# Performance work log

Measured on AMD Instinct MI355X. Metric: run time of the kernel, lower is better.

Reference implementation:

```python
import jax, jax.numpy as jnp
import numpy as np

# dims: B=batch, CIN/COUT=channels, T=timesteps, K=kernel length (= T+1, since
# max_timesteps=2048 is even and CKConv bumps it to odd), DK=SIREN hidden width
B, CIN, COUT, T, DK = 32, 32, 32, 2048, 32
K = T + 1


def setup_inputs() -> dict:
    key = jax.random.key(0)
    ks = jax.random.split(key, 9)
    u = lambda k, shape, lim: jax.random.uniform(k, shape, minval=-lim, maxval=lim)
    # SIREN layer 1 (Conv1d 1->DK, k=1): first layer init uniform(-1, 1)
    w1 = u(ks[0], (DK, 1), 1.0)
    b1 = u(ks[1], (DK,), 1.0)          # torch bias init: U(-1/sqrt(fan_in)), fan_in=1
    # SIREN layer 2 (DK->DK): uniform(-sqrt(6/DK)/omega0, +), omega0=1
    siren_val = float(np.sqrt(6.0 / DK))
    w2 = u(ks[2], (DK, DK), siren_val)
    b2 = u(ks[3], (DK,), float(1.0 / np.sqrt(DK)))
    # output layer (DK -> CIN*COUT)
    w3 = u(ks[4], (CIN * COUT, DK), siren_val)
    b3 = u(ks[5], (CIN * COUT,), float(1.0 / np.sqrt(DK)))
    omega1 = jnp.asarray(1.0, jnp.float32)
    omega2 = jnp.asarray(1.0, jnp.float32)
    bias = jax.random.normal(ks[6], (COUT,), jnp.float32)   # CKConv output bias
    x = jax.random.normal(ks[7], (B, CIN, T), jnp.float32)
    rel_pos = jnp.linspace(-1.0, 1.0, K, dtype=jnp.float32)  # buffer _rel_positions
    return dict(x=x, rel_pos=rel_pos, w1=w1, b1=b1, omega1=omega1,
                w2=w2, b2=b2, omega2=omega2, w3=w3, b3=b3, bias=bias)


def reference(x, rel_pos, w1, b1, omega1, w2, b2, omega2, w3, b3, bias):
    # --- SIREN kernel network: 1x1 convs over the K positions == matmuls ---
    pos = rel_pos[None, :]                                   # (1, K)
    h = jnp.sin(omega1 * (w1 @ pos + b1[:, None]))           # (DK, K)
    h = jnp.sin(omega2 * (w2 @ h + b2[:, None]))             # (DK, K)
    kern = (w3 @ h + b3[:, None]).reshape(COUT, CIN, K)      # (COUT, CIN, K)
    # --- causal conv: left-pad by K-1 zeros, then valid cross-correlation ---
    out = jax.lax.conv_general_dilated(
        x, kern, window_strides=(1,), padding=[(K - 1, 0)],
        dimension_numbers=("NCH", "OIH", "NCH"))             # (B, COUT, T)
    return out + bias[None, :, None]
```

## Files before the change

### kernel.cpp

```cpp
#include <hip/hip_runtime.h>
#include <hip/hip_bf16.h>
#include <stdint.h>

typedef short bf16x8 __attribute__((ext_vector_type(8)));
typedef float f32x16 __attribute__((ext_vector_type(16)));

#define T 2048
#define KLEN 2049
#define DK 32
#define NCO 32
#define NCI 32
#define NB 32

#define GR 2216
#define SREF 2055
#define WT_CH 257
#define WT_ELEMS (NCI*WT_CH*NCO*8)
#define XR_ELEMS (NB*NCI*GR)

#define WT_OFF 0
#define XR_OFF (WT_ELEMS*2)
#define XRS_OFF (XR_OFF + XR_ELEMS*2)

#define CIB 400
#define CPYB 13376
#define BUFB 27264
#define RED_OFF (2*BUFB)
#define LDS_TOT (RED_OFF + 16384)

__global__ __launch_bounds__(256) void gen_w(
    const float* __restrict__ rel_pos,
    const float* __restrict__ w1, const float* __restrict__ b1, const float* __restrict__ om1,
    const float* __restrict__ w2, const float* __restrict__ b2, const float* __restrict__ om2,
    const float* __restrict__ w3, const float* __restrict__ b3,
    uint16_t* __restrict__ Wt)
{
    int d = blockIdx.x;
    int tid = threadIdx.x;
    if (d >= KLEN) {
        for (int r = 0; r < 4; ++r) {
            int coci = tid + 256*r;
            int co = coci >> 5, ci = coci & 31;
            Wt[(((ci*WT_CH + (d>>3))*NCO + co)<<3) + (d&7)] = 0;
        }
        return;
    }
    int kk = 2048 - d;
    float pos = rel_pos[kk];
    __shared__ float h1[DK];
    __shared__ float h2[DK];
    if (tid < DK) h1[tid] = sinf(om1[0]*(w1[tid]*pos + b1[tid]));
    __syncthreads();
    if (tid < DK) {
        float a = b2[tid];
        for (int j = 0; j < DK; ++j) a += w2[tid*DK+j]*h1[j];
        h2[tid] = sinf(om2[0]*a);
    }
    __syncthreads();
    for (int r = 0; r < 4; ++r) {
        int coci = tid + 256*r;
        float a = b3[coci];
        for (int j = 0; j < DK; ++j) a += w3[coci*DK+j]*h2[j];
        int co = coci >> 5, ci = coci & 31;
        __hip_bfloat16 hv = __float2bfloat16(a);
        Wt[(((ci*WT_CH + (d>>3))*NCO + co)<<3) + (d&7)] = *(uint16_t*)&hv;
    }
}

__global__ __launch_bounds__(256) void gen_x(const float* __restrict__ x,
                                             uint16_t* __restrict__ xr,
                                             uint16_t* __restrict__ xrs)
{
    int idx = blockIdx.x*256 + threadIdx.x;
    if (idx >= NB*NCI*GR) return;
    int row = idx / GR;
    int g = idx - row*GR;
    int s = SREF - g;
    float v  = (s  >= 0 && s  < T) ? x[row*T + s]  : 0.f;
    int s2 = s - 1;
    float v2 = (s2 >= 0 && s2 < T) ? x[row*T + s2] : 0.f;
    __hip_bfloat16 hv = __float2bfloat16(v);
    __hip_bfloat16 hv2 = __float2bfloat16(v2);
    xr[idx]  = *(uint16_t*)&hv;
    xrs[idx] = *(uint16_t*)&hv2;
}

__device__ __forceinline__ void gld16(const uint16_t* g, char* l)
{
    typedef const __attribute__((address_space(1))) uint32_t GU;
    typedef __attribute__((address_space(3))) uint32_t LU;
    __builtin_amdgcn_global_load_lds((GU*)g, (LU*)l, 16, 0, 0);
}

__global__ __launch_bounds__(512, 2) void conv(
    const uint16_t* __restrict__ Wt, const uint16_t* __restrict__ xr,
    const float* __restrict__ bias, float* __restrict__ out)
{
    __shared__ uint4 lds4[LDS_TOT/16];
    char* ldsb = (char*)lds4;
    float* red = (float*)(ldsb + RED_OFF);
    int tid = threadIdx.x;
    int p = blockIdx.x >> 5;
    int b = blockIdx.x & 31;
    int w = tid >> 6, lane = tid & 63, n = lane & 31, hi = lane >> 5;
    int cig = w;

    int srcE[4], dstC[4];
    #pragma unroll
    for (int k = 0; k < 4; ++k) {
        int idxbase = (k < 3) ? (k*512 + w*64) : (1536 + w*64);
        int cpy = idxbase >= 832;
        int j0 = idxbase - cpy*832;
        dstC[k] = cpy*CPYB + (j0 << 4);
        int j = j0 + lane;
        if (j < 800) {
            int ci = (j*2622) >> 16;
            int q  = j - ci*25;
            srcE[k] = (cpy ? XR_ELEMS : 0) + (b*NCI + ci)*GR + (q << 3);
        } else srcE[k] = 0;
    }

    int obase = 39 - n + (hi << 3);
    int par = obase & 1;
    int bbb = cig*CIB + par*CPYB + ((obase - par) << 1);

    for (int phase = 0; phase < 2; ++phase) {
        int th = phase ? (63 - (p << 2)) : ((p << 2) + 3);
        int u = (th - 1) >> 1;
        int g0base = 2016 - (th << 5);

        f32x16 acc0, acc1, acc2, acc3;
        #pragma unroll
        for (int r = 0; r < 16; ++r) { acc0[r]=0.f; acc1[r]=0.f; acc2[r]=0.f; acc3[r]=0.f; }

        #pragma unroll
        for (int k = 0; k < 3; ++k)
            gld16(xr + srcE[k] + g0base, ldsb + dstC[k]);
        if (w < 2)
            gld16(xr + srcE[3] + g0base, ldsb + dstC[3]);
        __syncthreads();

        for (int wi = 0; wi <= u; ++wi) {
            int cur = wi & 1;
            if (wi < u) {
                int g0n = g0base + ((wi + 1) << 6);
                char* bufn = ldsb + (cur ^ 1)*BUFB;
                #pragma unroll
                for (int k = 0; k < 3; ++k)
                    gld16(xr + srcE[k] + g0n, bufn + dstC[k]);
                if (w < 2)
                    gld16(xr + srcE[3] + g0n, bufn + dstC[3]);
            }
            bool full = (wi < u);
            int dcw = wi << 3;
            const char* rbase = ldsb + cur*BUFB + bbb;

            #pragma unroll
            for (int cii = 0; cii < 4; ++cii) {
                int ci = (cii << 3) + cig;
                const uint16_t* aB = Wt + (((ci*WT_CH + dcw + hi)*NCO + n) << 3);
                bf16x8 av0 = *(const bf16x8*)(aB);
                bf16x8 av1 = *(const bf16x8*)(aB + 512);
                bf16x8 av2 = *(const bf16x8*)(aB + 1024);
                bf16x8 av3 = *(const bf16x8*)(aB + 1536);
                const char* pbase = rbase + cii*(8*CIB);

                #define RDBB(MM) union { uint32_t u_[4]; bf16x8 v; } bb; { \
                    const char* pp = pbase + ((MM) << 5); \
                    bb.u_[0] = *(const uint32_t*)(pp); \
                    bb.u_[1] = *(const uint32_t*)(pp + 4); \
                    bb.u_[2] = *(const uint32_t*)(pp + 8); \
                    bb.u_[3] = *(const uint32_t*)(pp + 12); }

                { RDBB(0) acc0 = __builtin_amdgcn_mfma_f32_32x32x16_bf16(av0, bb.v, acc0, 0,0,0); }
                { RDBB(1) acc0 = __builtin_amdgcn_mfma_f32_32x32x16_bf16(av1, bb.v, acc0, 0,0,0); }
                { RDBB(2) acc0 = __builtin_amdgcn_mfma_f32_32x32x16_bf16(av2, bb.v, acc0, 0,0,0);
                          acc1 = __builtin_amdgcn_mfma_f32_32x32x16_bf16(av0, bb.v, acc1, 0,0,0); }
                { RDBB(3) acc0 = __builtin_amdgcn_mfma_f32_32x32x16_bf16(av3, bb.v, acc0, 0,0,0);
                          acc1 = __builtin_amdgcn_mfma_f32_32x32x16_bf16(av1, bb.v, acc1, 0,0,0); }
                { RDBB(4) acc1 = __builtin_amdgcn_mfma_f32_32x32x16_bf16(av2, bb.v, acc1, 0,0,0);
                  if (full) acc2 = __builtin_amdgcn_mfma_f32_32x32x16_bf16(av0, bb.v, acc2, 0,0,0); }
                { RDBB(5) acc1 = __builtin_amdgcn_mfma_f32_32x32x16_bf16(av3, bb.v, acc1, 0,0,0);
                  if (full) acc2 = __builtin_amdgcn_mfma_f32_32x32x16_bf16(av1, bb.v, acc2, 0,0,0); }
                if (full) {
                    { RDBB(6) acc2 = __builtin_amdgcn_mfma_f32_32x32x16_bf16(av2, bb.v, acc2, 0,0,0);
                              acc3 = __builtin_amdgcn_mfma_f32_32x32x16_bf16(av0, bb.v, acc3, 0,0,0); }
                    { RDBB(7) acc2 = __builtin_amdgcn_mfma_f32_32x32x16_bf16(av3, bb.v, acc2, 0,0,0);
                              acc3 = __builtin_amdgcn_mfma_f32_32x32x16_bf16(av1, bb.v, acc3, 0,0,0); }
                    { RDBB(8) acc3 = __builtin_amdgcn_mfma_f32_32x32x16_bf16(av2, bb.v, acc3, 0,0,0); }
                    { RDBB(9) acc3 = __builtin_amdgcn_mfma_f32_32x32x16_bf16(av3, bb.v, acc3, 0,0,0); }
                }
                #undef RDBB
            }
            __syncthreads();
        }

        #pragma unroll
        for (int dlt = 0; dlt < 4; ++dlt) {
            f32x16 a = (dlt == 0) ? acc0 : (dlt == 1) ? acc1 : (dlt == 2) ? acc2 : acc3;
            __syncthreads();
            if (w < 4) {
                #pragma unroll
                for (int r = 0; r < 16; ++r)
                    red[(w*16 + r)*64 + lane] = a[r];
            }
            __syncthreads();
            if (w >= 4) {
                #pragma unroll
                for (int r = 0; r < 16; ++r)
                    red[((w-4)*16 + r)*64 + lane] += a[r];
            }
            __syncthreads();
            int t0 = (th - dlt) << 5;
            #pragma unroll
            for (int h = 0; h < 2; ++h) {
                int e = tid + (h << 9);
                int lane_e = e & 63;
                int reg = e >> 6;
                float s = 0.f;
                #pragma unroll
                for (int ww = 0; ww < 4; ++ww) s += red[(ww*16 + reg)*64 + lane_e];
                int co = (reg & 3) + ((reg >> 2) << 3) + ((lane_e >> 5) << 2);
                int t = t0 + (lane_e & 31);
                out[(b*NCO + co)*T + t] = s + bias[co];
            }
        }
        __syncthreads();
    }
}

extern "C" void kernel_launch(void* const* d_in, const int* in_sizes, int n_in,
                              void* d_out, int out_size, void* d_ws, size_t ws_size,
                              hipStream_t stream)
{
    const float* x       = (const float*)d_in[0];
    const float* rel_pos = (const float*)d_in[1];
    const float* w1  = (const float*)d_in[2];
    const float* b1  = (const float*)d_in[3];
    const float* om1 = (const float*)d_in[4];
    const float* w2  = (const float*)d_in[5];
    const float* b2  = (const float*)d_in[6];
    const float* om2 = (const float*)d_in[7];
    const float* w3  = (const float*)d_in[8];
    const float* b3  = (const float*)d_in[9];
    const float* bias = (const float*)d_in[10];
    float* out = (float*)d_out;
    char* ws = (char*)d_ws;
    uint16_t* Wt  = (uint16_t*)(ws + WT_OFF);
    uint16_t* xrp = (uint16_t*)(ws + XR_OFF);
    uint16_t* xrs = (uint16_t*)(ws + XRS_OFF);

    hipLaunchKernelGGL(gen_w, dim3(WT_CH*8), dim3(256), 0, stream,
                       rel_pos, w1, b1, om1, w2, b2, om2, w3, b3, Wt);
    int n2 = NB*NCI*GR;
    hipLaunchKernelGGL(gen_x, dim3((n2+255)/256), dim3(256), 0, stream, x, xrp, xrs);
    hipLaunchKernelGGL(conv, dim3(NB*8), dim3(512), 0, stream, Wt, xrp, bias, out);
}
```

Before: 179.6 us.

## Split conv phases into separate blocks and prefetch next weight fragments

Each block used to handle two time tiles (a short and a long one) in sequence. Now each phase is its own block, which doubles the grid to 512 blocks, and launch bounds rise to 4 blocks per SM to allow higher occupancy. Inside the inner loop, the A-operand weight loads for the next input-channel group are issued before the current MFMA chain to hide global latency. The price is more register pressure under the tighter launch bound, possible spills, and load imbalance, since each block's work now differs widely with its time position.

```diff
diff --git a/kernel.cpp b/kernel.cpp
--- a/kernel.cpp
+++ b/kernel.cpp
@@ -92,7 +92,7 @@
     __builtin_amdgcn_global_load_lds((GU*)g, (LU*)l, 16, 0, 0);
 }
 
-__global__ __launch_bounds__(512, 2) void conv(
+__global__ __launch_bounds__(512, 4) void conv(
     const uint16_t* __restrict__ Wt, const uint16_t* __restrict__ xr,
     const float* __restrict__ bias, float* __restrict__ out)
 {
@@ -100,8 +100,12 @@
     char* ldsb = (char*)lds4;
     float* red = (float*)(ldsb + RED_OFF);
     int tid = threadIdx.x;
-    int p = blockIdx.x >> 5;
     int b = blockIdx.x & 31;
+    int q = blockIdx.x >> 5;
+    int p = q & 7;
+    int th = (q < 8) ? (63 - (p << 2)) : ((p << 2) + 3);
+    int u = (th - 1) >> 1;
+    int g0base = 2016 - (th << 5);
     int w = tid >> 6, lane = tid & 63, n = lane & 31, hi = lane >> 5;
     int cig = w;
 
@@ -115,8 +119,8 @@
         int j = j0 + lane;
         if (j < 800) {
             int ci = (j*2622) >> 16;
-            int q  = j - ci*25;
-            srcE[k] = (cpy ? XR_ELEMS : 0) + (b*NCI + ci)*GR + (q << 3);
+            int qq = j - ci*25;
+            srcE[k] = (cpy ? XR_ELEMS : 0) + (b*NCI + ci)*GR + (qq << 3);
         } else srcE[k] = 0;
     }
 
@@ -124,108 +128,111 @@
     int par = obase & 1;
     int bbb = cig*CIB + par*CPYB + ((obase - par) << 1);
 
-    for (int phase = 0; phase < 2; ++phase) {
-        int th = phase ? (63 - (p << 2)) : ((p << 2) + 3);
-        int u = (th - 1) >> 1;
-        int g0base = 2016 - (th << 5);
-
-        f32x16 acc0, acc1, acc2, acc3;
+    f32x16 acc0, acc1, acc2, acc3;
+    #pragma unroll
+    for (int r = 0; r < 16; ++r) { acc0[r]=0.f; acc1[r]=0.f; acc2[r]=0.f; acc3[r]=0.f; }
+
+    #pragma unroll
+    for (int k = 0; k < 3; ++k)
+        gld16(xr + srcE[k] + g0base, ldsb + dstC[k]);
+    if (w < 2)
+        gld16(xr + srcE[3] + g0base, ldsb + dstC[3]);
+    __syncthreads();
+
+    for (int wi = 0; wi <= u; ++wi) {
+        int cur = wi & 1;
+        if (wi < u) {
+            int g0n = g0base + ((wi + 1) << 6);
+            char* bufn = ldsb + (cur ^ 1)*BUFB;
+            #pragma unroll
+            for (int k = 0; k < 3; ++k)
+                gld16(xr + srcE[k] + g0n, bufn + dstC[k]);
+            if (w < 2)
+                gld16(xr + srcE[3] + g0n, bufn + dstC[3]);
+        }
+        bool full = (wi < u);
+        int dcw = wi << 3;
+        const char* rbase = ldsb + cur*BUFB + bbb;
+
+        bf16x8 av0, av1, av2, av3, nv0, nv1, nv2, nv3;
+        {
+            const uint16_t* aB = Wt + (((cig*WT_CH + dcw + hi)*NCO + n) << 3);
+            av0 = *(const bf16x8*)(aB);
+            av1 = *(const bf16x8*)(aB + 512);
+            av2 = *(const bf16x8*)(aB + 1024);
+            av3 = *(const bf16x8*)(aB + 1536);
+        }
         #pragma unroll
-        for (int r = 0; r < 16; ++r) { acc0[r]=0.f; acc1[r]=0.f; acc2[r]=0.f; acc3[r]=0.f; }
-
+        for (int cii = 0; cii < 4; ++cii) {
+            if (cii < 3) {
+                const uint16_t* aN = Wt + (((((cii+1)*8 + cig)*WT_CH + dcw + hi)*NCO + n) << 3);
+                nv0 = *(const bf16x8*)(aN);
+                nv1 = *(const bf16x8*)(aN + 512);
+                nv2 = *(const bf16x8*)(aN + 1024);
+                nv3 = *(const bf16x8*)(aN + 1536);
+            }
+            const char* pbase = rbase + cii*(8*CIB);
+
+            #define RDBB(MM) union { uint32_t u_[4]; bf16x8 v; } bb; { \
+                const char* pp = pbase + ((MM) << 5); \
+                bb.u_[0] = *(const uint32_t*)(pp); \
+                bb.u_[1] = *(const uint32_t*)(pp + 4); \
+                bb.u_[2] = *(const uint32_t*)(pp + 8); \
+                bb.u_[3] = *(const uint32_t*)(pp + 12); }
+
+            { RDBB(0) acc0 = __builtin_amdgcn_mfma_f32_32x32x16_bf16(av0, bb.v, acc0, 0,0,0); }
+            { RDBB(1) acc0 = __builtin_amdgcn_mfma_f32_32x32x16_bf16(av1, bb.v, acc0, 0,0,0); }
+            { RDBB(2) acc0 = __builtin_amdgcn_mfma_f32_32x32x16_bf16(av2, bb.v, acc0, 0,0,0);
+                      acc1 = __builtin_amdgcn_mfma_f32_32x32x16_bf16(av0, bb.v, acc1, 0,0,0); }
+            { RDBB(3) acc0 = __builtin_amdgcn_mfma_f32_32x32x16_bf16(av3, bb.v, acc0, 0,0,0);
+                      acc1 = __builtin_amdgcn_mfma_f32_32x32x16_bf16(av1, bb.v, acc1, 0,0,0); }
+            { RDBB(4) acc1 = __builtin_amdgcn_mfma_f32_32x32x16_bf16(av2, bb.v, acc1, 0,0,0);
+              if (full) acc2 = __builtin_amdgcn_mfma_f32_32x32x16_bf16(av0, bb.v, acc2, 0,0,0); }
+            { RDBB(5) acc1 = __builtin_amdgcn_mfma_f32_32x32x16_bf16(av3, bb.v, acc1, 0,0,0);
+              if (full) acc2 = __builtin_amdgcn_mfma_f32_32x32x16_bf16(av1, bb.v, acc2, 0,0,0); }
+            if (full) {
+                { RDBB(6) acc2 = __builtin_amdgcn_mfma_f32_32x32x16_bf16(av2, bb.v, acc2, 0,0,0);
+                          acc3 = __builtin_amdgcn_mfma_f32_32x32x16_bf16(av0, bb.v, acc3, 0,0,0); }
+                { RDBB(7) acc2 = __builtin_amdgcn_mfma_f32_32x32x16_bf16(av3, bb.v, acc2, 0,0,0);
+                          acc3 = __builtin_amdgcn_mfma_f32_32x32x16_bf16(av1, bb.v, acc3, 0,0,0); }
+                { RDBB(8) acc3 = __builtin_amdgcn_mfma_f32_32x32x16_bf16(av2, bb.v, acc3, 0,0,0); }
+                { RDBB(9) acc3 = __builtin_amdgcn_mfma_f32_32x32x16_bf16(av3, bb.v, acc3, 0,0,0); }
+            }
+            #undef RDBB
+            if (cii < 3) { av0 = nv0; av1 = nv1; av2 = nv2; av3 = nv3; }
+        }
+        __syncthreads();
+    }
+
+    #pragma unroll
+    for (int dlt = 0; dlt < 4; ++dlt) {
+        f32x16 a = (dlt == 0) ? acc0 : (dlt == 1) ? acc1 : (dlt == 2) ? acc2 : acc3;
+        __syncthreads();
+        if (w < 4) {
+            #pragma unroll
+            for (int r = 0; r < 16; ++r)
+                red[(w*16 + r)*64 + lane] = a[r];
+        }
+        __syncthreads();
+        if (w >= 4) {
+            #pragma unroll
+            for (int r = 0; r < 16; ++r)
+                red[((w-4)*16 + r)*64 + lane] += a[r];
+        }
+        __syncthreads();
+        int t0 = (th - dlt) << 5;
         #pragma unroll
-        for (int k = 0; k < 3; ++k)
-            gld16(xr + srcE[k] + g0base, ldsb + dstC[k]);
-        if (w < 2)
-            gld16(xr + srcE[3] + g0base, ldsb + dstC[3]);
-        __syncthreads();
-
-        for (int wi = 0; wi <= u; ++wi) {
-            int cur = wi & 1;
-            if (wi < u) {
-                int g0n = g0base + ((wi + 1) << 6);
-                char* bufn = ldsb + (cur ^ 1)*BUFB;
-                #pragma unroll
-                for (int k = 0; k < 3; ++k)
-                    gld16(xr + srcE[k] + g0n, bufn + dstC[k]);
-                if (w < 2)
-                    gld16(xr + srcE[3] + g0n, bufn + dstC[3]);
-            }
-            bool full = (wi < u);
-            int dcw = wi << 3;
-            const char* rbase = ldsb + cur*BUFB + bbb;
-
-            #pragma unroll
-            for (int cii = 0; cii < 4; ++cii) {
-                int ci = (cii << 3) + cig;
-                const uint16_t* aB = Wt + (((ci*WT_CH + dcw + hi)*NCO + n) << 3);
-                bf16x8 av0 = *(const bf16x8*)(aB);
-                bf16x8 av1 = *(const bf16x8*)(aB + 512);
-                bf16x8 av2 = *(const bf16x8*)(aB + 1024);
-                bf16x8 av3 = *(const bf16x8*)(aB + 1536);
-                const char* pbase = rbase + cii*(8*CIB);
-
-                #define RDBB(MM) union { uint32_t u_[4]; bf16x8 v; } bb; { \
-                    const char* pp = pbase + ((MM) << 5); \
-                    bb.u_[0] = *(const uint32_t*)(pp); \
-                    bb.u_[1] = *(const uint32_t*)(pp + 4); \
-                    bb.u_[2] = *(const uint32_t*)(pp + 8); \
-                    bb.u_[3] = *(const uint32_t*)(pp + 12); }
-
-                { RDBB(0) acc0 = __builtin_amdgcn_mfma_f32_32x32x16_bf16(av0, bb.v, acc0, 0,0,0); }
-                { RDBB(1) acc0 = __builtin_amdgcn_mfma_f32_32x32x16_bf16(av1, bb.v, acc0, 0,0,0); }
-                { RDBB(2) acc0 = __builtin_amdgcn_mfma_f32_32x32x16_bf16(av2, bb.v, acc0, 0,0,0);
-                          acc1 = __builtin_amdgcn_mfma_f32_32x32x16_bf16(av0, bb.v, acc1, 0,0,0); }
-                { RDBB(3) acc0 = __builtin_amdgcn_mfma_f32_32x32x16_bf16(av3, bb.v, acc0, 0,0,0);
-                          acc1 = __builtin_amdgcn_mfma_f32_32x32x16_bf16(av1, bb.v, acc1, 0,0,0); }
-                { RDBB(4) acc1 = __builtin_amdgcn_mfma_f32_32x32x16_bf16(av2, bb.v, acc1, 0,0,0);
-                  if (full) acc2 = __builtin_amdgcn_mfma_f32_32x32x16_bf16(av0, bb.v, acc2, 0,0,0); }
-                { RDBB(5) acc1 = __builtin_amdgcn_mfma_f32_32x32x16_bf16(av3, bb.v, acc1, 0,0,0);
-                  if (full) acc2 = __builtin_amdgcn_mfma_f32_32x32x16_bf16(av1, bb.v, acc2, 0,0,0); }
-                if (full) {
-                    { RDBB(6) acc2 = __builtin_amdgcn_mfma_f32_32x32x16_bf16(av2, bb.v, acc2, 0,0,0);
-                              acc3 = __builtin_amdgcn_mfma_f32_32x32x16_bf16(av0, bb.v, acc3, 0,0,0); }
-                    { RDBB(7) acc2 = __builtin_amdgcn_mfma_f32_32x32x16_bf16(av3, bb.v, acc2, 0,0,0);
-                              acc3 = __builtin_amdgcn_mfma_f32_32x32x16_bf16(av1, bb.v, acc3, 0,0,0); }
-                    { RDBB(8) acc3 = __builtin_amdgcn_mfma_f32_32x32x16_bf16(av2, bb.v, acc3, 0,0,0); }
-                    { RDBB(9) acc3 = __builtin_amdgcn_mfma_f32_32x32x16_bf16(av3, bb.v, acc3, 0,0,0); }
-                }
-                #undef RDBB
-            }
-            __syncthreads();
-        }
-
-        #pragma unroll
-        for (int dlt = 0; dlt < 4; ++dlt) {
-            f32x16 a = (dlt == 0) ? acc0 : (dlt == 1) ? acc1 : (dlt == 2) ? acc2 : acc3;
-            __syncthreads();
-            if (w < 4) {
-                #pragma unroll
-                for (int r = 0; r < 16; ++r)
-                    red[(w*16 + r)*64 + lane] = a[r];
-            }
-            __syncthreads();
-            if (w >= 4) {
-                #pragma unroll
-                for (int r = 0; r < 16; ++r)
-                    red[((w-4)*16 + r)*64 + lane] += a[r];
-            }
-            __syncthreads();
-            int t0 = (th - dlt) << 5;
-            #pragma unroll
-            for (int h = 0; h < 2; ++h) {
-                int e = tid + (h << 9);
-                int lane_e = e & 63;
-                int reg = e >> 6;
-                float s = 0.f;
-                #pragma unroll
-                for (int ww = 0; ww < 4; ++ww) s += red[(ww*16 + reg)*64 + lane_e];
-                int co = (reg & 3) + ((reg >> 2) << 3) + ((lane_e >> 5) << 2);
-                int t = t0 + (lane_e & 31);
-                out[(b*NCO + co)*T + t] = s + bias[co];
-            }
-        }
-        __syncthreads();
+        for (int h = 0; h < 2; ++h) {
+            int e = tid + (h << 9);
+            int lane_e = e & 63;
+            int reg = e >> 6;
+            float s = 0.f;
+            #pragma unroll
+            for (int ww = 0; ww < 4; ++ww) s += red[(ww*16 + reg)*64 + lane_e];
+            int co = (reg & 3) + ((reg >> 2) << 3) + ((lane_e >> 5) << 2);
+            int t = t0 + (lane_e & 31);
+            out[(b*NCO + co)*T + t] = s + bias[co];
+        }
     }
 }
 
@@ -254,5 +261,5 @@
                        rel_pos, w1, b1, om1, w2, b2, om2, w3, b3, Wt);
     int n2 = NB*NCI*GR;
     hipLaunchKernelGGL(gen_x, dim3((n2+255)/256), dim3(256), 0, stream, x, xrp, xrs);
-    hipLaunchKernelGGL(conv, dim3(NB*8), dim3(512), 0, stream, Wt, xrp, bias, out);
-}
+    hipLaunchKernelGGL(conv, dim3(NB*16), dim3(512), 0, stream, Wt, xrp, bias, out);
+}
```

After: 181.5 us. No clear change (+1.1%).

## Widen causal-conv K-window per stage and split phases into separate blocks

Applied to the files above, without the earlier changes.

The conv kernel now stages twice the lag window per pipeline step (128 instead of 64 positions, 8 weight fragments per ci) and reuses each A fragment across four accumulator tiles with a longer MFMA chain. The two triangular phases that used to run sequentially in one block now go to separate blocks, doubling the grid to 512. The reduction buffer aliases the staging LDS, and launch bounds ask for 4 blocks per CU. The aim is fewer barriers and loop iterations per MFMA and more parallelism. The cost is a larger LDS footprint, more VGPR pressure from the extra A fragments, and some wasted MFMAs on the partial last window.

```diff
diff --git a/kernel.cpp b/kernel.cpp
--- a/kernel.cpp
+++ b/kernel.cpp
@@ -22,11 +22,12 @@
 #define XR_OFF (WT_ELEMS*2)
 #define XRS_OFF (XR_OFF + XR_ELEMS*2)
 
-#define CIB 400
-#define CPYB 13376
-#define BUFB 27264
-#define RED_OFF (2*BUFB)
-#define LDS_TOT (RED_OFF + 16384)
+#define CIB 528
+#define GPC 1056
+#define GPCP 1088
+#define CPYB 17472
+#define BUFB (2*CPYB)
+#define LDS_TOT (2*BUFB)
 
 __global__ __launch_bounds__(256) void gen_w(
     const float* __restrict__ rel_pos,
@@ -92,140 +93,137 @@
     __builtin_amdgcn_global_load_lds((GU*)g, (LU*)l, 16, 0, 0);
 }
 
-__global__ __launch_bounds__(512, 2) void conv(
+__global__ __launch_bounds__(512, 4) void conv(
     const uint16_t* __restrict__ Wt, const uint16_t* __restrict__ xr,
     const float* __restrict__ bias, float* __restrict__ out)
 {
     __shared__ uint4 lds4[LDS_TOT/16];
     char* ldsb = (char*)lds4;
-    float* red = (float*)(ldsb + RED_OFF);
+    float* red = (float*)lds4;
     int tid = threadIdx.x;
-    int p = blockIdx.x >> 5;
     int b = blockIdx.x & 31;
+    int q = blockIdx.x >> 5;
+    int p = q & 7;
+    int th = (q < 8) ? (63 - (p << 2)) : ((p << 2) + 3);
+    int nw = (th + 1) >> 2;
+    int g0base = 2016 - (th << 5);
     int w = tid >> 6, lane = tid & 63, n = lane & 31, hi = lane >> 5;
     int cig = w;
 
-    int srcE[4], dstC[4];
+    int srcE[5], dstC[5];
     #pragma unroll
-    for (int k = 0; k < 4; ++k) {
-        int idxbase = (k < 3) ? (k*512 + w*64) : (1536 + w*64);
-        int cpy = idxbase >= 832;
-        int j0 = idxbase - cpy*832;
-        dstC[k] = cpy*CPYB + (j0 << 4);
-        int j = j0 + lane;
-        if (j < 800) {
-            int ci = (j*2622) >> 16;
-            int q  = j - ci*25;
-            srcE[k] = (cpy ? XR_ELEMS : 0) + (b*NCI + ci)*GR + (q << 3);
-        } else srcE[k] = 0;
+    for (int k = 0; k < 5; ++k) {
+        int gi = tid + (k << 9);
+        if (gi < 2176) {
+            int cpy = gi >= GPCP;
+            int j = gi - cpy*GPCP;
+            dstC[k] = cpy*CPYB + (j << 4);
+            if (j < GPC) {
+                int ci = (j*1986) >> 16;
+                int qq = j - ci*33;
+                srcE[k] = (cpy ? XR_ELEMS : 0) + (b*NCI + ci)*GR + (qq << 3);
+            } else srcE[k] = 0;
+        } else { srcE[k] = 0; dstC[k] = -1; }
     }
 
     int obase = 39 - n + (hi << 3);
     int par = obase & 1;
     int bbb = cig*CIB + par*CPYB + ((obase - par) << 1);
 
-    for (int phase = 0; phase < 2; ++phase) {
-        int th = phase ? (63 - (p << 2)) : ((p << 2) + 3);
-        int u = (th - 1) >> 1;
-        int g0base = 2016 - (th << 5);
-
-        f32x16 acc0, acc1, acc2, acc3;
+    f32x16 acc0, acc1, acc2, acc3;
+    #pragma unroll
+    for (int r = 0; r < 16; ++r) { acc0[r]=0.f; acc1[r]=0.f; acc2[r]=0.f; acc3[r]=0.f; }
+
+    #define STAGE(BUF, GOFF) { \
+        _Pragma("unroll") \
+        for (int k = 0; k < 5; ++k) \
+            if (dstC[k] >= 0) gld16(xr + srcE[k] + (GOFF), (BUF) + dstC[k]); }
+
+    STAGE(ldsb, g0base)
+    __syncthreads();
+
+    for (int wi = 0; wi < nw; ++wi) {
+        int cur = wi & 1;
+        if (wi + 1 < nw) {
+            char* bufn = ldsb + (cur ^ 1)*BUFB;
+            int g0n = g0base + ((wi + 1) << 7);
+            STAGE(bufn, g0n)
+        }
+        int dcw = wi << 4;
+        const char* rbase = ldsb + cur*BUFB + bbb;
+
         #pragma unroll
-        for (int r = 0; r < 16; ++r) { acc0[r]=0.f; acc1[r]=0.f; acc2[r]=0.f; acc3[r]=0.f; }
-
+        for (int cii = 0; cii < 4; ++cii) {
+            int ci = (cii << 3) + cig;
+            const uint16_t* aB = Wt + (((ci*WT_CH + dcw + hi)*NCO + n) << 3);
+            bf16x8 av0 = *(const bf16x8*)(aB);
+            bf16x8 av1 = *(const bf16x8*)(aB + 512);
+            bf16x8 av2 = *(const bf16x8*)(aB + 1024);
+            bf16x8 av3 = *(const bf16x8*)(aB + 1536);
+            bf16x8 av4 = *(const bf16x8*)(aB + 2048);
+            bf16x8 av5 = *(const bf16x8*)(aB + 2560);
+            bf16x8 av6 = *(const bf16x8*)(aB + 3072);
+            bf16x8 av7 = *(const bf16x8*)(aB + 3584);
+            const char* pbase = rbase + cii*(8*CIB);
+
+            #define RDBB(MM) union { uint32_t u_[4]; bf16x8 v; } bb; { \
+                const char* pp = pbase + ((MM) << 5); \
+                bb.u_[0] = *(const uint32_t*)(pp); \
+                bb.u_[1] = *(const uint32_t*)(pp + 4); \
+                bb.u_[2] = *(const uint32_t*)(pp + 8); \
+                bb.u_[3] = *(const uint32_t*)(pp + 12); }
+            #define MF(AC, AV) AC = __builtin_amdgcn_mfma_f32_32x32x16_bf16(AV, bb.v, AC, 0,0,0);
+
+            { RDBB(0)  MF(acc0, av0) }
+            { RDBB(1)  MF(acc0, av1) }
+            { RDBB(2)  MF(acc0, av2) MF(acc1, av0) }
+            { RDBB(3)  MF(acc0, av3) MF(acc1, av1) }
+            { RDBB(4)  MF(acc0, av4) MF(acc1, av2) MF(acc2, av0) }
+            { RDBB(5)  MF(acc0, av5) MF(acc1, av3) MF(acc2, av1) }
+            { RDBB(6)  MF(acc0, av6) MF(acc1, av4) MF(acc2, av2) MF(acc3, av0) }
+            { RDBB(7)  MF(acc0, av7) MF(acc1, av5) MF(acc2, av3) MF(acc3, av1) }
+            { RDBB(8)  MF(acc1, av6) MF(acc2, av4) MF(acc3, av2) }
+            { RDBB(9)  MF(acc1, av7) MF(acc2, av5) MF(acc3, av3) }
+            { RDBB(10) MF(acc2, av6) MF(acc3, av4) }
+            { RDBB(11) MF(acc2, av7) MF(acc3, av5) }
+            { RDBB(12) MF(acc3, av6) }
+            { RDBB(13) MF(acc3, av7) }
+            #undef MF
+            #undef RDBB
+        }
+        __syncthreads();
+    }
+    #undef STAGE
+
+    #pragma unroll
+    for (int dlt = 0; dlt < 4; ++dlt) {
+        f32x16 a = (dlt == 0) ? acc0 : (dlt == 1) ? acc1 : (dlt == 2) ? acc2 : acc3;
+        __syncthreads();
+        if (w < 4) {
+            #pragma unroll
+            for (int r = 0; r < 16; ++r)
+                red[(w*16 + r)*64 + lane] = a[r];
+        }
+        __syncthreads();
+        if (w >= 4) {
+            #pragma unroll
+            for (int r = 0; r < 16; ++r)
+                red[((w-4)*16 + r)*64 + lane] += a[r];
+        }
+        __syncthreads();
+        int t0 = (th - dlt) << 5;
         #pragma unroll
-        for (int k = 0; k < 3; ++k)
-            gld16(xr + srcE[k] + g0base, ldsb + dstC[k]);
-        if (w < 2)
-            gld16(xr + srcE[3] + g0base, ldsb + dstC[3]);
-        __syncthreads();
-
-        for (int wi = 0; wi <= u; ++wi) {
-            int cur = wi & 1;
-            if (wi < u) {
-                int g0n = g0base + ((wi + 1) << 6);
-                char* bufn = ldsb + (cur ^ 1)*BUFB;
-                #pragma unroll
-                for (int k = 0; k < 3; ++k)
-                    gld16(xr + srcE[k] + g0n, bufn + dstC[k]);
-                if (w < 2)
-                    gld16(xr + srcE[3] + g0n, bufn + dstC[3]);
-            }
-            bool full = (wi < u);
-            int dcw = wi << 3;
-            const char* rbase = ldsb + cur*BUFB + bbb;
-
+        for (int h = 0; h < 2; ++h) {
+            int e = tid + (h << 9);
+            int lane_e = e & 63;
+            int reg = e >> 6;
+            float s = 0.f;
             #pragma unroll
-            for (int cii = 0; cii < 4; ++cii) {
-                int ci = (cii << 3) + cig;
-                const uint16_t* aB = Wt + (((ci*WT_CH + dcw + hi)*NCO + n) << 3);
-                bf16x8 av0 = *(const bf16x8*)(aB);
-                bf16x8 av1 = *(const bf16x8*)(aB + 512);
-                bf16x8 av2 = *(const bf16x8*)(aB + 1024);
-                bf16x8 av3 = *(const bf16x8*)(aB + 1536);
-                const char* pbase = rbase + cii*(8*CIB);
-
-                #define RDBB(MM) union { uint32_t u_[4]; bf16x8 v; } bb; { \
-                    const char* pp = pbase + ((MM) << 5); \
-                    bb.u_[0] = *(const uint32_t*)(pp); \
-                    bb.u_[1] = *(const uint32_t*)(pp + 4); \
-                    bb.u_[2] = *(const uint32_t*)(pp + 8); \
-                    bb.u_[3] = *(const uint32_t*)(pp + 12); }
-
-                { RDBB(0) acc0 = __builtin_amdgcn_mfma_f32_32x32x16_bf16(av0, bb.v, acc0, 0,0,0); }
-                { RDBB(1) acc0 = __builtin_amdgcn_mfma_f32_32x32x16_bf16(av1, bb.v, acc0, 0,0,0); }
-                { RDBB(2) acc0 = __builtin_amdgcn_mfma_f32_32x32x16_bf16(av2, bb.v, acc0, 0,0,0);
-                          acc1 = __builtin_amdgcn_mfma_f32_32x32x16_bf16(av0, bb.v, acc1, 0,0,0); }
-                { RDBB(3) acc0 = __builtin_amdgcn_mfma_f32_32x32x16_bf16(av3, bb.v, acc0, 0,0,0);
-                          acc1 = __builtin_amdgcn_mfma_f32_32x32x16_bf16(av1, bb.v, acc1, 0,0,0); }
-                { RDBB(4) acc1 = __builtin_amdgcn_mfma_f32_32x32x16_bf16(av2, bb.v, acc1, 0,0,0);
-                  if (full) acc2 = __builtin_amdgcn_mfma_f32_32x32x16_bf16(av0, bb.v, acc2, 0,0,0); }
-                { RDBB(5) acc1 = __builtin_amdgcn_mfma_f32_32x32x16_bf16(av3, bb.v, acc1, 0,0,0);
-                  if (full) acc2 = __builtin_amdgcn_mfma_f32_32x32x16_bf16(av1, bb.v, acc2, 0,0,0); }
-                if (full) {
-                    { RDBB(6) acc2 = __builtin_amdgcn_mfma_f32_32x32x16_bf16(av2, bb.v, acc2, 0,0,0);
-                              acc3 = __builtin_amdgcn_mfma_f32_32x32x16_bf16(av0, bb.v, acc3, 0,0,0); }
-                    { RDBB(7) acc2 = __builtin_amdgcn_mfma_f32_32x32x16_bf16(av3, bb.v, acc2, 0,0,0);
-                              acc3 = __builtin_amdgcn_mfma_f32_32x32x16_bf16(av1, bb.v, acc3, 0,0,0); }
-                    { RDBB(8) acc3 = __builtin_amdgcn_mfma_f32_32x32x16_bf16(av2, bb.v, acc3, 0,0,0); }
-                    { RDBB(9) acc3 = __builtin_amdgcn_mfma_f32_32x32x16_bf16(av3, bb.v, acc3, 0,0,0); }
-                }
-                #undef RDBB
-            }
-            __syncthreads();
-        }
-
-        #pragma unroll
-        for (int dlt = 0; dlt < 4; ++dlt) {
-            f32x16 a = (dlt == 0) ? acc0 : (dlt == 1) ? acc1 : (dlt == 2) ? acc2 : acc3;
-            __syncthreads();
-            if (w < 4) {
-                #pragma unroll
-                for (int r = 0; r < 16; ++r)
-                    red[(w*16 + r)*64 + lane] = a[r];
-            }
-            __syncthreads();
-            if (w >= 4) {
-                #pragma unroll
-                for (int r = 0; r < 16; ++r)
-                    red[((w-4)*16 + r)*64 + lane] += a[r];
-            }
-            __syncthreads();
-            int t0 = (th - dlt) << 5;
-            #pragma unroll
-            for (int h = 0; h < 2; ++h) {
-                int e = tid + (h << 9);
-                int lane_e = e & 63;
-                int reg = e >> 6;
-                float s = 0.f;
-                #pragma unroll
-                for (int ww = 0; ww < 4; ++ww) s += red[(ww*16 + reg)*64 + lane_e];
-                int co = (reg & 3) + ((reg >> 2) << 3) + ((lane_e >> 5) << 2);
-                int t = t0 + (lane_e & 31);
-                out[(b*NCO + co)*T + t] = s + bias[co];
-            }
-        }
-        __syncthreads();
+            for (int ww = 0; ww < 4; ++ww) s += red[(ww*16 + reg)*64 + lane_e];
+            int co = (reg & 3) + ((reg >> 2) << 3) + ((lane_e >> 5) << 2);
+            int t = t0 + (lane_e & 31);
+            out[(b*NCO + co)*T + t] = s + bias[co];
+        }
     }
 }
 
@@ -254,5 +252,5 @@
                        rel_pos, w1, b1, om1, w2, b2, om2, w3, b3, Wt);
     int n2 = NB*NCI*GR;
     hipLaunchKernelGGL(gen_x, dim3((n2+255)/256), dim3(256), 0, stream, x, xrp, xrs);
-    hipLaunchKernelGGL(conv, dim3(NB*8), dim3(512), 0, stream, Wt, xrp, bias, out);
-}
+    hipLaunchKernelGGL(conv, dim3(NB*16), dim3(512), 0, stream, Wt, xrp, bias, out);
+}
```

Result: faster. 167.4 us (-6.8%).
